# Kernel tuning notes

Measured on AMD Instinct MI355X. Metric: run time of the kernel, lower is better.

The kernel has to match this reference:

```python
import jax, jax.numpy as jnp
import numpy as np

N_USERS = 100000
N_ITEMS = 50000
N = N_USERS + N_ITEMS
EMB = 64
NNZ = 8000000
N_LAYERS = 3


def setup_inputs() -> dict:
    key = jax.random.key(0)
    k1, k2, k3, k4, k5 = jax.random.split(key, 5)
    user_emb = jax.random.normal(k1, (N_USERS, EMB), dtype=jnp.float32) * 0.1
    item_emb = jax.random.normal(k2, (N_ITEMS, EMB), dtype=jnp.float32) * 0.1
    adj_rows = jax.random.randint(k3, (NNZ,), 0, N, dtype=jnp.int32)
    adj_cols = jax.random.randint(k4, (NNZ,), 0, N, dtype=jnp.int32)
    # normalized-adjacency-like small positive values
    adj_vals = jax.random.uniform(k5, (NNZ,), dtype=jnp.float32) * 0.01
    return {
        "user_emb": user_emb,
        "item_emb": item_emb,
        "adj_rows": adj_rows,
        "adj_cols": adj_cols,
        "adj_vals": adj_vals,
    }


def spmm(rows, cols, vals, x):
    # sparse [N,N] @ dense [N,d]: gather source rows, scale, scatter-add to dest
    msgs = vals[:, None] * x[cols]          # [nnz, d]
    return jax.ops.segment_sum(msgs, rows, num_segments=N)  # [N, d]


def reference(user_emb, item_emb, adj_rows, adj_cols, adj_vals):
    ego = jnp.concatenate([user_emb, item_emb], axis=0)  # [N, d]
    acc = ego  # running sum of layer outputs (fused stack+mean)
    for _ in range(N_LAYERS):
        ego = spmm(adj_rows, adj_cols, adj_vals, ego)
        acc = acc + ego
    all_embeddings = acc / jnp.float32(N_LAYERS + 1)
    return all_embeddings[:N_USERS], all_embeddings[N_USERS:]
```

## Files before the change

kernel.cpp:

```cpp
#include <hip/hip_runtime.h>

#define N_USERS 100000
#define N_ITEMS 50000
#define N_TOTAL 150000
#define EMB 64
#define NNZ_CONST 8000000

#define CB_SHIFT 8
#define ROWS_PER_CB 256
#define NCB 586
#define CAP_R 14592
#define EPB 8192

#define VAL_ENC 1638400.0f
#define VAL_DEC 2.3841858e-9f
#define FP8_SCALE 256.0f

typedef unsigned char u8;
typedef unsigned short u16;
typedef unsigned int u32;
typedef unsigned long long u64;
typedef float v2f __attribute__((ext_vector_type(2)));

__device__ __forceinline__ u16 f32_to_bf16(float f) {
    u32 b = __float_as_uint(f);
    b += 0x7FFFu + ((b >> 16) & 1u);
    return (u16)(b >> 16);
}
__device__ __forceinline__ float bf16lo_to_f32(u32 w) {
    return __uint_as_float(w << 16);
}
__device__ __forceinline__ float bf16hi_to_f32(u32 w) {
    return __uint_as_float(w & 0xFFFF0000u);
}
__device__ __forceinline__ u32 pack_bf16x2(float lo, float hi) {
    return ((u32)f32_to_bf16(hi) << 16) | f32_to_bf16(lo);
}
__device__ __forceinline__ u32 pack_fp8x4(float a, float b, float c, float d) {
    u32 r = (u32)__builtin_amdgcn_cvt_pk_fp8_f32(a, b, 0, false);
    r = (u32)__builtin_amdgcn_cvt_pk_fp8_f32(c, d, (int)r, true);
    return r;
}

__global__ void lgcn_init_kernel(const float* __restrict__ user_emb,
                                 const float* __restrict__ item_emb,
                                 float* __restrict__ acc,
                                 u8* __restrict__ ego8) {
    const long total4 = (long)N_TOTAL * EMB / 4;
    long idx = (long)blockIdx.x * blockDim.x + threadIdx.x;
    if (idx >= total4) return;
    long e = idx * 4;
    const long user_elems = (long)N_USERS * EMB;
    float4 v;
    if (e < user_elems) {
        v = *(const float4*)(user_emb + e);
    } else {
        v = *(const float4*)(item_emb + (e - user_elems));
    }
    *(float4*)(acc + e) = v;
    *(u32*)(ego8 + e) = pack_fp8x4(v.x * FP8_SCALE, v.y * FP8_SCALE,
                                   v.z * FP8_SCALE, v.w * FP8_SCALE);
}

__global__ void lgcn_gcinit_kernel(int* __restrict__ gcursor) {
    int t = blockIdx.x * blockDim.x + threadIdx.x;
    if (t < NCB) gcursor[t] = t * CAP_R;
}

__global__ void __launch_bounds__(512) lgcn_part_kernel(
        const int* __restrict__ rows,
        const int* __restrict__ cols,
        const float* __restrict__ vals,
        int* __restrict__ gcursor,
        u32* __restrict__ pairs,
        u8* __restrict__ rl8) {
    __shared__ u32 stage32[EPB];
    __shared__ u8  stage8[EPB];
    __shared__ int lhist[NCB];
    __shared__ int loffs[NCB + 1];
    __shared__ int lcur[NCB];
    __shared__ int gres[NCB];
    const int t = threadIdx.x;
    const long base = (long)blockIdx.x * EPB;
    long rem = (long)NNZ_CONST - base;
    const int n = (rem < EPB) ? (int)rem : EPB;
    const int n4 = n >> 2;

    for (int i = t; i < NCB; i += 512) lhist[i] = 0;
    __syncthreads();

    for (int i4 = t; i4 < n4; i4 += 512) {
        int4 r = *(const int4*)(rows + base + (long)i4 * 4);
        atomicAdd(&lhist[r.x >> CB_SHIFT], 1);
        atomicAdd(&lhist[r.y >> CB_SHIFT], 1);
        atomicAdd(&lhist[r.z >> CB_SHIFT], 1);
        atomicAdd(&lhist[r.w >> CB_SHIFT], 1);
    }
    __syncthreads();

    if (t < 64) {
        int loc[10];
        int s = 0;
        #pragma unroll
        for (int k = 0; k < 10; ++k) {
            int i = t * 10 + k;
            loc[k] = (i < NCB) ? lhist[i] : 0;
            s += loc[k];
        }
        int inc = s;
        #pragma unroll
        for (int d = 1; d < 64; d <<= 1) {
            int u = __shfl_up(inc, d, 64);
            if (t >= d) inc += u;
        }
        int ex = inc - s;
        #pragma unroll
        for (int k = 0; k < 10; ++k) {
            int i = t * 10 + k;
            if (i < NCB) { loffs[i] = ex; lcur[i] = ex; ex += loc[k]; }
        }
        if (t == 63) loffs[NCB] = ex;
    }
    __syncthreads();

    for (int i = t; i < NCB; i += 512) {
        int c = lhist[i];
        gres[i] = c ? atomicAdd(&gcursor[i], c) : 0;
    }
    __syncthreads();

    for (int i4 = t; i4 < n4; i4 += 512) {
        int4 r = *(const int4*)(rows + base + (long)i4 * 4);
        int4 c = *(const int4*)(cols + base + (long)i4 * 4);
        float4 v = *(const float4*)(vals + base + (long)i4 * 4);
#define PUTL(RR, CC, VV)                                                \
        {                                                               \
            const int cb = (RR) >> CB_SHIFT;                            \
            int pos = atomicAdd(&lcur[cb], 1);                          \
            int k14 = (int)((VV) * VAL_ENC + 0.5f);                     \
            if (k14 > 16383) k14 = 16383;                               \
            stage32[pos] = ((u32)k14 << 18) | (u32)(CC);                \
            stage8[pos] = (u8)((RR) & (ROWS_PER_CB - 1));               \
        }
        PUTL(r.x, c.x, v.x)
        PUTL(r.y, c.y, v.y)
        PUTL(r.z, c.z, v.z)
        PUTL(r.w, c.w, v.w)
#undef PUTL
    }
    __syncthreads();

    for (int i = t; i < n; i += 512) {
        int lo = 0, hi = NCB;
        while (hi - lo > 1) {
            int mid = (lo + hi) >> 1;
            if (loffs[mid] <= i) lo = mid; else hi = mid;
        }
        long d = (long)gres[lo] + (i - loffs[lo]);
        pairs[d] = stage32[i];
        rl8[d] = stage8[i];
    }
}

__global__ void __launch_bounds__(512) lgcn_csort_kernel(
        const int* __restrict__ gcursor,
        const u8* __restrict__ rl8,
        u32* __restrict__ pairs,
        int2* __restrict__ row_rng) {
    __shared__ u32 stage[CAP_R];
    __shared__ int rhist[ROWS_PER_CB];
    __shared__ int roffs[ROWS_PER_CB + 1];
    __shared__ int rcur[ROWS_PER_CB];
    const int b = blockIdx.x;
    const int t = threadIdx.x;
    const long gbase = (long)b * CAP_R;
    int n = gcursor[b] - (int)gbase;
    if (n < 0) n = 0;
    if (n > CAP_R) n = CAP_R;

    if (t < ROWS_PER_CB) rhist[t] = 0;
    __syncthreads();

    for (int i = t; i < n; i += 512)
        atomicAdd(&rhist[rl8[gbase + i]], 1);
    __syncthreads();

    if (t < 64) {
        int l0 = rhist[t * 4 + 0], l1 = rhist[t * 4 + 1];
        int l2 = rhist[t * 4 + 2], l3 = rhist[t * 4 + 3];
        int s = l0 + l1 + l2 + l3;
        int inc = s;
        #pragma unroll
        for (int d = 1; d < 64; d <<= 1) {
            int u = __shfl_up(inc, d, 64);
            if (t >= d) inc += u;
        }
        int ex = inc - s;
        roffs[t * 4 + 0] = ex;
        roffs[t * 4 + 1] = ex + l0;
        roffs[t * 4 + 2] = ex + l0 + l1;
        roffs[t * 4 + 3] = ex + l0 + l1 + l2;
        rcur[t * 4 + 0] = ex;
        rcur[t * 4 + 1] = ex + l0;
        rcur[t * 4 + 2] = ex + l0 + l1;
        rcur[t * 4 + 3] = ex + l0 + l1 + l2;
        if (t == 63) roffs[ROWS_PER_CB] = ex + s;
    }
    __syncthreads();

    if (t < ROWS_PER_CB) {
        int grow = b * ROWS_PER_CB + t;
        if (grow < N_TOTAL)
            row_rng[grow] = make_int2((int)gbase + roffs[t],
                                      (int)gbase + roffs[t + 1]);
    }

    for (int i = t; i < n; i += 512) {
        int rl = rl8[gbase + i];
        int pos = atomicAdd(&rcur[rl], 1);
        stage[pos] = pairs[gbase + i];
    }
    __syncthreads();

    for (int i = t; i < n; i += 512)
        pairs[gbase + i] = stage[i];
}

template <bool WFP8>
__global__ void lgcn_spmm_kernel(const int2* __restrict__ row_rng,
                                 const u32* __restrict__ pairs,
                                 const u8* __restrict__ src8,
                                 u8* __restrict__ dst8,
                                 u16* __restrict__ dst_bf16) {
    const int lane = threadIdx.x & 63;
    const int g   = (lane >> 3) & 1;
    const int l8  = lane & 7;
    const int row = blockIdx.x * 16 + (threadIdx.x >> 4);
    if (row >= N_TOTAL) return;
    const int2 rng = row_rng[row];
    const int start = rng.x;
    const int end   = rng.y;

    const u8* srcl = src8 + l8 * 8;

    v2f qa0 = {0.f, 0.f}, qa1 = {0.f, 0.f}, qa2 = {0.f, 0.f}, qa3 = {0.f, 0.f};
    v2f qb0 = {0.f, 0.f}, qb1 = {0.f, 0.f}, qb2 = {0.f, 0.f}, qb3 = {0.f, 0.f};

#define PROC(E, Q0, Q1, Q2, Q3)                                             \
    {                                                                       \
        const u32 p = __builtin_nontemporal_load(&pairs[E]);                \
        const int   c = (int)(p & 0x3FFFFu);                                \
        const float v = (float)(p >> 18) * VAL_DEC;                         \
        const uint2 x = *(const uint2*)(srcl + ((size_t)c << 6));           \
        const v2f vv = {v, v};                                              \
        Q0 += vv * __builtin_amdgcn_cvt_pk_f32_fp8(x.x, false);             \
        Q1 += vv * __builtin_amdgcn_cvt_pk_f32_fp8(x.x, true);              \
        Q2 += vv * __builtin_amdgcn_cvt_pk_f32_fp8(x.y, false);             \
        Q3 += vv * __builtin_amdgcn_cvt_pk_f32_fp8(x.y, true);              \
    }

    int e = start + g;
    for (; e + 6 < end; e += 8) {
        PROC(e,     qa0, qa1, qa2, qa3)
        PROC(e + 2, qb0, qb1, qb2, qb3)
        PROC(e + 4, qa0, qa1, qa2, qa3)
        PROC(e + 6, qb0, qb1, qb2, qb3)
    }
    for (; e < end; e += 2) {
        PROC(e, qa0, qa1, qa2, qa3)
    }
#undef PROC
    qa0 += qb0; qa1 += qb1; qa2 += qb2; qa3 += qb3;

    float s0 = qa0.x, s1 = qa0.y, s2 = qa1.x, s3 = qa1.y;
    float s4 = qa2.x, s5 = qa2.y, s6 = qa3.x, s7 = qa3.y;
    s0 += __shfl_xor(s0, 8); s1 += __shfl_xor(s1, 8);
    s2 += __shfl_xor(s2, 8); s3 += __shfl_xor(s3, 8);
    s4 += __shfl_xor(s4, 8); s5 += __shfl_xor(s5, 8);
    s6 += __shfl_xor(s6, 8); s7 += __shfl_xor(s7, 8);

    if (g == 0) {
        const size_t o = (size_t)row * EMB + l8 * 8;
        uint2 h0, h1;
        h0.x = pack_bf16x2(s0, s1);
        h0.y = pack_bf16x2(s2, s3);
        h1.x = pack_bf16x2(s4, s5);
        h1.y = pack_bf16x2(s6, s7);
        *(uint2*)(dst_bf16 + o) = h0;
        *(uint2*)(dst_bf16 + o + 4) = h1;
        if (WFP8) {
            uint2 q;
            q.x = pack_fp8x4(s0 * FP8_SCALE, s1 * FP8_SCALE,
                             s2 * FP8_SCALE, s3 * FP8_SCALE);
            q.y = pack_fp8x4(s4 * FP8_SCALE, s5 * FP8_SCALE,
                             s6 * FP8_SCALE, s7 * FP8_SCALE);
            *(uint2*)(dst8 + o) = q;
        }
    }
}

__global__ void lgcn_merge_kernel(float* __restrict__ acc,
                                  const u16* __restrict__ e1,
                                  const u16* __restrict__ e2,
                                  const u16* __restrict__ e3) {
    const long total8 = (long)N_TOTAL * EMB / 8;
    long idx = (long)blockIdx.x * blockDim.x + threadIdx.x;
    if (idx >= total8) return;
    long o = idx * 8;
    float4 x0 = *(const float4*)(acc + o);
    float4 x1 = *(const float4*)(acc + o + 4);
    const uint4 h1 = *(const uint4*)(e1 + o);
    const uint4 h2 = *(const uint4*)(e2 + o);
    const uint4 h3 = *(const uint4*)(e3 + o);
    x0.x = (x0.x + bf16lo_to_f32(h1.x) + bf16lo_to_f32(h2.x) + bf16lo_to_f32(h3.x)) * 0.25f;
    x0.y = (x0.y + bf16hi_to_f32(h1.x) + bf16hi_to_f32(h2.x) + bf16hi_to_f32(h3.x)) * 0.25f;
    x0.z = (x0.z + bf16lo_to_f32(h1.y) + bf16lo_to_f32(h2.y) + bf16lo_to_f32(h3.y)) * 0.25f;
    x0.w = (x0.w + bf16hi_to_f32(h1.y) + bf16hi_to_f32(h2.y) + bf16hi_to_f32(h3.y)) * 0.25f;
    x1.x = (x1.x + bf16lo_to_f32(h1.z) + bf16lo_to_f32(h2.z) + bf16lo_to_f32(h3.z)) * 0.25f;
    x1.y = (x1.y + bf16hi_to_f32(h1.z) + bf16hi_to_f32(h2.z) + bf16hi_to_f32(h3.z)) * 0.25f;
    x1.z = (x1.z + bf16lo_to_f32(h1.w) + bf16lo_to_f32(h2.w) + bf16lo_to_f32(h3.w)) * 0.25f;
    x1.w = (x1.w + bf16hi_to_f32(h1.w) + bf16hi_to_f32(h2.w) + bf16hi_to_f32(h3.w)) * 0.25f;
    *(float4*)(acc + o) = x0;
    *(float4*)(acc + o + 4) = x1;
}

extern "C" void kernel_launch(void* const* d_in, const int* in_sizes, int n_in,
                              void* d_out, int out_size, void* d_ws, size_t ws_size,
                              hipStream_t stream) {
    const float* user_emb = (const float*)d_in[0];
    const float* item_emb = (const float*)d_in[1];
    const int*   adj_rows = (const int*)d_in[2];
    const int*   adj_cols = (const int*)d_in[3];
    const float* adj_vals = (const float*)d_in[4];

    float* acc = (float*)d_out;

    char* ws = (char*)d_ws;
    u8* fp8A = (u8*)ws;             ws += (size_t)N_TOTAL * EMB;
    u8* fp8B = (u8*)ws;             ws += (size_t)N_TOTAL * EMB;
    u16* e1 = (u16*)ws;             ws += (size_t)N_TOTAL * EMB * 2;
    u16* e2 = (u16*)ws;             ws += (size_t)N_TOTAL * EMB * 2;
    u16* e3 = (u16*)ws;             ws += (size_t)N_TOTAL * EMB * 2;
    u32* pairs = (u32*)ws;          ws += (size_t)NCB * CAP_R * 4;
    u8* rl8 = (u8*)ws;              ws += (size_t)NCB * CAP_R;
    int2* row_rng = (int2*)ws;      ws += (size_t)(N_TOTAL + 16) * 8;
    int* gcursor = (int*)ws;        ws += (size_t)(NCB + 8) * 4;

    const int block = 256;
    const long total4 = (long)N_TOTAL * EMB / 4;
    const int grid_elem = (int)((total4 + block - 1) / block);

    lgcn_init_kernel<<<grid_elem, block, 0, stream>>>(user_emb, item_emb, acc, fp8A);

    lgcn_gcinit_kernel<<<(NCB + 255) / 256, 256, 0, stream>>>(gcursor);
    const int grid_part = (NNZ_CONST + EPB - 1) / EPB;
    lgcn_part_kernel<<<grid_part, 512, 0, stream>>>(adj_rows, adj_cols, adj_vals,
                                                    gcursor, pairs, rl8);
    lgcn_csort_kernel<<<NCB, 512, 0, stream>>>(gcursor, rl8, pairs, row_rng);

    const int grid_spmm = (N_TOTAL + 15) / 16;
    lgcn_spmm_kernel<true><<<grid_spmm, block, 0, stream>>>(row_rng, pairs, fp8A, fp8B, e1);
    lgcn_spmm_kernel<true><<<grid_spmm, block, 0, stream>>>(row_rng, pairs, fp8B, fp8A, e2);
    lgcn_spmm_kernel<false><<<grid_spmm, block, 0, stream>>>(row_rng, pairs, fp8A, fp8B, e3);

    const long total8 = (long)N_TOTAL * EMB / 8;
    const int grid_merge = (int)((total8 + block - 1) / block);
    lgcn_merge_kernel<<<grid_merge, block, 0, stream>>>(acc, e1, e2, e3);
}
```

Before: 508.3 us.

## Sort edges by column chunk within row blocks and accumulate SpMM in LDS

The counting sort now keys each edge by (source column chunk, local row), so each 256-row block's edges are grouped into five column ranges. The SpMM becomes one block per 256-row bucket with a 64 KB LDS accumulator. All threads walk one column chunk at a time with a barrier between chunks, aiming to keep the gathered fp8 source rows (about 2 MB per chunk) resident in cache. This lowers parallelism to 586 blocks with heavy LDS use and can cause load imbalance, since each 8-lane group handles 8 rows serially.

```diff
diff --git a/kernel.cpp b/kernel.cpp
--- a/kernel.cpp
+++ b/kernel.cpp
@@ -11,6 +11,11 @@
 #define NCB 586
 #define CAP_R 14592
 #define EPB 8192
+
+#define CHUNK_SHIFT 15
+#define NCHUNK 5
+#define KBINS (NCHUNK * ROWS_PER_CB)
+#define CRNG_STRIDE 1312
 
 #define VAL_ENC 1638400.0f
 #define VAL_DEC 2.3841858e-9f
@@ -166,29 +171,37 @@
         const int* __restrict__ gcursor,
         const u8* __restrict__ rl8,
         u32* __restrict__ pairs,
-        int2* __restrict__ row_rng) {
+        int* __restrict__ crng) {
     __shared__ u32 stage[CAP_R];
-    __shared__ int rhist[ROWS_PER_CB];
-    __shared__ int roffs[ROWS_PER_CB + 1];
-    __shared__ int rcur[ROWS_PER_CB];
+    __shared__ int khist[KBINS];
+    __shared__ int kcur[KBINS];
     const int b = blockIdx.x;
     const int t = threadIdx.x;
     const long gbase = (long)b * CAP_R;
+    const int cbase = b * CRNG_STRIDE;
     int n = gcursor[b] - (int)gbase;
     if (n < 0) n = 0;
     if (n > CAP_R) n = CAP_R;
 
-    if (t < ROWS_PER_CB) rhist[t] = 0;
-    __syncthreads();
-
-    for (int i = t; i < n; i += 512)
-        atomicAdd(&rhist[rl8[gbase + i]], 1);
+    for (int i = t; i < KBINS; i += 512) khist[i] = 0;
+    __syncthreads();
+
+    for (int i = t; i < n; i += 512) {
+        u32 p = pairs[gbase + i];
+        int key = (int)((p & 0x3FFFFu) >> CHUNK_SHIFT) * ROWS_PER_CB
+                + (int)rl8[gbase + i];
+        atomicAdd(&khist[key], 1);
+    }
     __syncthreads();
 
     if (t < 64) {
-        int l0 = rhist[t * 4 + 0], l1 = rhist[t * 4 + 1];
-        int l2 = rhist[t * 4 + 2], l3 = rhist[t * 4 + 3];
-        int s = l0 + l1 + l2 + l3;
+        int loc[20];
+        int s = 0;
+        #pragma unroll
+        for (int k = 0; k < 20; ++k) {
+            loc[k] = khist[t * 20 + k];
+            s += loc[k];
+        }
         int inc = s;
         #pragma unroll
         for (int d = 1; d < 64; d <<= 1) {
@@ -196,29 +209,22 @@
             if (t >= d) inc += u;
         }
         int ex = inc - s;
-        roffs[t * 4 + 0] = ex;
-        roffs[t * 4 + 1] = ex + l0;
-        roffs[t * 4 + 2] = ex + l0 + l1;
-        roffs[t * 4 + 3] = ex + l0 + l1 + l2;
-        rcur[t * 4 + 0] = ex;
-        rcur[t * 4 + 1] = ex + l0;
-        rcur[t * 4 + 2] = ex + l0 + l1;
-        rcur[t * 4 + 3] = ex + l0 + l1 + l2;
-        if (t == 63) roffs[ROWS_PER_CB] = ex + s;
-    }
-    __syncthreads();
-
-    if (t < ROWS_PER_CB) {
-        int grow = b * ROWS_PER_CB + t;
-        if (grow < N_TOTAL)
-            row_rng[grow] = make_int2((int)gbase + roffs[t],
-                                      (int)gbase + roffs[t + 1]);
-    }
+        #pragma unroll
+        for (int k = 0; k < 20; ++k) {
+            kcur[t * 20 + k] = ex;
+            crng[cbase + t * 20 + k] = (int)gbase + ex;
+            ex += loc[k];
+        }
+        if (t == 63) crng[cbase + KBINS] = (int)gbase + ex;
+    }
+    __syncthreads();
 
     for (int i = t; i < n; i += 512) {
-        int rl = rl8[gbase + i];
-        int pos = atomicAdd(&rcur[rl], 1);
-        stage[pos] = pairs[gbase + i];
+        u32 p = pairs[gbase + i];
+        int key = (int)((p & 0x3FFFFu) >> CHUNK_SHIFT) * ROWS_PER_CB
+                + (int)rl8[gbase + i];
+        int pos = atomicAdd(&kcur[key], 1);
+        stage[pos] = p;
     }
     __syncthreads();
 
@@ -227,73 +233,87 @@
 }
 
 template <bool WFP8>
-__global__ void lgcn_spmm_kernel(const int2* __restrict__ row_rng,
-                                 const u32* __restrict__ pairs,
-                                 const u8* __restrict__ src8,
-                                 u8* __restrict__ dst8,
-                                 u16* __restrict__ dst_bf16) {
-    const int lane = threadIdx.x & 63;
-    const int g   = (lane >> 3) & 1;
-    const int l8  = lane & 7;
-    const int row = blockIdx.x * 16 + (threadIdx.x >> 4);
-    if (row >= N_TOTAL) return;
-    const int2 rng = row_rng[row];
-    const int start = rng.x;
-    const int end   = rng.y;
-
+__global__ void __launch_bounds__(256) lgcn_spmm_kernel(
+        const int* __restrict__ crng,
+        const u32* __restrict__ pairs,
+        const u8* __restrict__ src8,
+        u8* __restrict__ dst8,
+        u16* __restrict__ dst_bf16) {
+    __shared__ float lacc[ROWS_PER_CB * EMB];
+    const int t = threadIdx.x;
+    const int b = blockIdx.x;
+    for (int i = t; i < ROWS_PER_CB * EMB / 4; i += 256)
+        ((float4*)lacc)[i] = make_float4(0.f, 0.f, 0.f, 0.f);
+    __syncthreads();
+
+    const int g  = t >> 3;
+    const int l8 = t & 7;
     const u8* srcl = src8 + l8 * 8;
-
-    v2f qa0 = {0.f, 0.f}, qa1 = {0.f, 0.f}, qa2 = {0.f, 0.f}, qa3 = {0.f, 0.f};
-    v2f qb0 = {0.f, 0.f}, qb1 = {0.f, 0.f}, qb2 = {0.f, 0.f}, qb3 = {0.f, 0.f};
-
-#define PROC(E, Q0, Q1, Q2, Q3)                                             \
+    const int cbase = b * CRNG_STRIDE;
+
+#define PROC(E)                                                             \
     {                                                                       \
         const u32 p = __builtin_nontemporal_load(&pairs[E]);                \
         const int   c = (int)(p & 0x3FFFFu);                                \
         const float v = (float)(p >> 18) * VAL_DEC;                         \
         const uint2 x = *(const uint2*)(srcl + ((size_t)c << 6));           \
         const v2f vv = {v, v};                                              \
-        Q0 += vv * __builtin_amdgcn_cvt_pk_f32_fp8(x.x, false);             \
-        Q1 += vv * __builtin_amdgcn_cvt_pk_f32_fp8(x.x, true);              \
-        Q2 += vv * __builtin_amdgcn_cvt_pk_f32_fp8(x.y, false);             \
-        Q3 += vv * __builtin_amdgcn_cvt_pk_f32_fp8(x.y, true);              \
-    }
-
-    int e = start + g;
-    for (; e + 6 < end; e += 8) {
-        PROC(e,     qa0, qa1, qa2, qa3)
-        PROC(e + 2, qb0, qb1, qb2, qb3)
-        PROC(e + 4, qa0, qa1, qa2, qa3)
-        PROC(e + 6, qb0, qb1, qb2, qb3)
-    }
-    for (; e < end; e += 2) {
-        PROC(e, qa0, qa1, qa2, qa3)
+        q0 += vv * __builtin_amdgcn_cvt_pk_f32_fp8(x.x, false);             \
+        q1 += vv * __builtin_amdgcn_cvt_pk_f32_fp8(x.x, true);              \
+        q2 += vv * __builtin_amdgcn_cvt_pk_f32_fp8(x.y, false);             \
+        q3 += vv * __builtin_amdgcn_cvt_pk_f32_fp8(x.y, true);              \
+    }
+
+    for (int k = 0; k < NCHUNK; ++k) {
+        #pragma unroll
+        for (int j = 0; j < 8; ++j) {
+            const int row = g + 32 * j;
+            const int key = (k << 8) | row;
+            const int s  = crng[cbase + key];
+            const int e2 = crng[cbase + key + 1];
+            v2f q0 = {0.f, 0.f}, q1 = {0.f, 0.f};
+            v2f q2 = {0.f, 0.f}, q3 = {0.f, 0.f};
+            int e = s;
+            for (; e + 3 < e2; e += 4) {
+                PROC(e) PROC(e + 1) PROC(e + 2) PROC(e + 3)
+            }
+            for (; e < e2; ++e) PROC(e)
+            if (s < e2) {
+                float* lp = lacc + row * EMB + l8 * 8;
+                float4 p0 = *(float4*)lp;
+                float4 p1 = *(float4*)(lp + 4);
+                p0.x += q0.x; p0.y += q0.y; p0.z += q1.x; p0.w += q1.y;
+                p1.x += q2.x; p1.y += q2.y; p1.z += q3.x; p1.w += q3.y;
+                *(float4*)lp = p0;
+                *(float4*)(lp + 4) = p1;
+            }
+        }
+        __syncthreads();
     }
 #undef PROC
-    qa0 += qb0; qa1 += qb1; qa2 += qb2; qa3 += qb3;
-
-    float s0 = qa0.x, s1 = qa0.y, s2 = qa1.x, s3 = qa1.y;
-    float s4 = qa2.x, s5 = qa2.y, s6 = qa3.x, s7 = qa3.y;
-    s0 += __shfl_xor(s0, 8); s1 += __shfl_xor(s1, 8);
-    s2 += __shfl_xor(s2, 8); s3 += __shfl_xor(s3, 8);
-    s4 += __shfl_xor(s4, 8); s5 += __shfl_xor(s5, 8);
-    s6 += __shfl_xor(s6, 8); s7 += __shfl_xor(s7, 8);
-
-    if (g == 0) {
-        const size_t o = (size_t)row * EMB + l8 * 8;
-        uint2 h0, h1;
-        h0.x = pack_bf16x2(s0, s1);
-        h0.y = pack_bf16x2(s2, s3);
-        h1.x = pack_bf16x2(s4, s5);
-        h1.y = pack_bf16x2(s6, s7);
-        *(uint2*)(dst_bf16 + o) = h0;
-        *(uint2*)(dst_bf16 + o + 4) = h1;
+
+    const int rowbase = b * ROWS_PER_CB;
+    for (int i = t; i < ROWS_PER_CB * 8; i += 256) {
+        const int row = i >> 3;
+        const int d8 = i & 7;
+        const int grow = rowbase + row;
+        if (grow >= N_TOTAL) continue;
+        const float* lp = lacc + row * EMB + d8 * 8;
+        const float4 p0 = *(const float4*)lp;
+        const float4 p1 = *(const float4*)(lp + 4);
+        const size_t o = (size_t)grow * EMB + d8 * 8;
+        uint4 h;
+        h.x = pack_bf16x2(p0.x, p0.y);
+        h.y = pack_bf16x2(p0.z, p0.w);
+        h.z = pack_bf16x2(p1.x, p1.y);
+        h.w = pack_bf16x2(p1.z, p1.w);
+        *(uint4*)(dst_bf16 + o) = h;
         if (WFP8) {
             uint2 q;
-            q.x = pack_fp8x4(s0 * FP8_SCALE, s1 * FP8_SCALE,
-                             s2 * FP8_SCALE, s3 * FP8_SCALE);
-            q.y = pack_fp8x4(s4 * FP8_SCALE, s5 * FP8_SCALE,
-                             s6 * FP8_SCALE, s7 * FP8_SCALE);
+            q.x = pack_fp8x4(p0.x * FP8_SCALE, p0.y * FP8_SCALE,
+                             p0.z * FP8_SCALE, p0.w * FP8_SCALE);
+            q.y = pack_fp8x4(p1.x * FP8_SCALE, p1.y * FP8_SCALE,
+                             p1.z * FP8_SCALE, p1.w * FP8_SCALE);
             *(uint2*)(dst8 + o) = q;
         }
     }
@@ -343,7 +363,7 @@
     u16* e3 = (u16*)ws;             ws += (size_t)N_TOTAL * EMB * 2;
     u32* pairs = (u32*)ws;          ws += (size_t)NCB * CAP_R * 4;
     u8* rl8 = (u8*)ws;              ws += (size_t)NCB * CAP_R;
-    int2* row_rng = (int2*)ws;      ws += (size_t)(N_TOTAL + 16) * 8;
+    int* crng = (int*)ws;           ws += (size_t)NCB * CRNG_STRIDE * 4;
     int* gcursor = (int*)ws;        ws += (size_t)(NCB + 8) * 4;
 
     const int block = 256;
@@ -356,12 +376,11 @@
     const int grid_part = (NNZ_CONST + EPB - 1) / EPB;
     lgcn_part_kernel<<<grid_part, 512, 0, stream>>>(adj_rows, adj_cols, adj_vals,
                                                     gcursor, pairs, rl8);
-    lgcn_csort_kernel<<<NCB, 512, 0, stream>>>(gcursor, rl8, pairs, row_rng);
-
-    const int grid_spmm = (N_TOTAL + 15) / 16;
-    lgcn_spmm_kernel<true><<<grid_spmm, block, 0, stream>>>(row_rng, pairs, fp8A, fp8B, e1);
-    lgcn_spmm_kernel<true><<<grid_spmm, block, 0, stream>>>(row_rng, pairs, fp8B, fp8A, e2);
-    lgcn_spmm_kernel<false><<<grid_spmm, block, 0, stream>>>(row_rng, pairs, fp8A, fp8B, e3);
+    lgcn_csort_kernel<<<NCB, 512, 0, stream>>>(gcursor, rl8, pairs, crng);
+
+    lgcn_spmm_kernel<true><<<NCB, 256, 0, stream>>>(crng, pairs, fp8A, fp8B, e1);
+    lgcn_spmm_kernel<true><<<NCB, 256, 0, stream>>>(crng, pairs, fp8B, fp8A, e2);
+    lgcn_spmm_kernel<false><<<NCB, 256, 0, stream>>>(crng, pairs, fp8A, fp8B, e3);
 
     const long total8 = (long)N_TOTAL * EMB / 8;
     const int grid_merge = (int)((total8 + block - 1) / block);
```

Measured after the change: 1.223 ms. 2.41x slower.
